# Kernel tuning notes

Measured on AMD Instinct MI355X. Metric: run time of the kernel, lower is better.

Reference implementation:

```python
import jax, jax.numpy as jnp
import numpy as np

DT = 0.1
THRESH = 10.0

def setup_inputs() -> dict:
    key = jax.random.key(0)
    ks = jax.random.split(key, 6)
    B, S, H, V = 2, 1024, 1024, 50257
    hidden_states = jax.random.normal(ks[0], (B, S, H), dtype=jnp.float32)
    ttu_state = jnp.zeros((B, 3), dtype=jnp.float32)
    W_imp = jax.random.normal(ks[1], (3, H), dtype=jnp.float32) * 0.02
    b_imp = jnp.zeros((3,), dtype=jnp.float32)
    W_lm = jax.random.normal(ks[2], (V, H), dtype=jnp.float32) * 0.02
    W_mod = jax.random.normal(ks[3], (V, 3), dtype=jnp.float32) * 0.02
    # gamma, alpha_c, beta_c, delta, alpha_d, epsilon, alpha_m
    ttu_params = jax.random.uniform(ks[4], (7,), dtype=jnp.float32, minval=0.1, maxval=1.0)
    return {"hidden_states": hidden_states, "ttu_state": ttu_state,
            "W_imp": W_imp, "b_imp": b_imp, "W_lm": W_lm, "W_mod": W_mod,
            "ttu_params": ttu_params}

def _ttu_scan(ttu_state, impulses, ttu_params):
    # impulses: [S, B, 3] (time-major for scan)
    gamma, alpha_c, beta_c, delta, alpha_d, epsilon, alpha_m = ttu_params
    def step(state, imp):
        phi_c, phi_d, phi_m = state[:, 0], state[:, 1], state[:, 2]
        dphi_c = gamma * imp[:, 0] - alpha_c * phi_c - beta_c * phi_c * phi_d
        dphi_d = delta * phi_c ** 2 - alpha_d * phi_d
        dphi_m = epsilon * phi_d - alpha_m * phi_m
        new_c = phi_c + DT * dphi_c
        new_d = phi_d + DT * dphi_d
        new_m = phi_m + DT * dphi_m
        # saturation damping on phi_d
        new_d = jnp.where(jnp.abs(new_d) > THRESH, jnp.float32(0.5), jnp.float32(1.0)) * new_d
        new_state = jnp.stack([new_c, new_d, new_m], axis=1)  # [B, 3]
        return new_state, new_state
    return jax.lax.scan(step, ttu_state, impulses)

def reference(hidden_states, ttu_state, W_imp, b_imp, W_lm, W_mod, ttu_params):
    # impulse projections computed in batch up front: [S, B, 3]
    impulses = jnp.einsum('bsh,dh->sbd', hidden_states, W_imp) + b_imp
    final_state, states = _ttu_scan(ttu_state, impulses, ttu_params)  # states: [S, B, 3]
    # base lm logits + 0.1 * modulation from ttu trajectory
    logits = jnp.einsum('bsh,vh->bsv', hidden_states, W_lm) \
           + 0.1 * jnp.einsum('sbd,vd->bsv', states, W_mod)
    return logits, final_state
```

## Files before the change

kernel.cpp:

```cpp
#include <hip/hip_runtime.h>
#include <hip/hip_bf16.h>

typedef float  f32x4  __attribute__((ext_vector_type(4)));
typedef short  bf16x8 __attribute__((ext_vector_type(8)));
typedef short  bf16x4 __attribute__((ext_vector_type(4)));

typedef const void __attribute__((address_space(1))) gv_t;
typedef void __attribute__((address_space(3))) sv_t;

namespace {

constexpr int B_ = 2;
constexpr int S_ = 1024;
constexpr int H_ = 1024;
constexpr int V_ = 50257;
constexpr int M_ = B_ * S_;
constexpr int VP2_ = 50432;
constexpr int VP1_ = 50304;
constexpr float DT_ = 0.1f;
constexpr float THRESH_ = 10.0f;

constexpr int BK = 64;
constexpr int NT = H_ / BK;

__device__ __forceinline__ unsigned short f2bf(float f) {
  union { float f; unsigned u; } x;
  x.f = f;
  x.u += 0x7FFFu + ((x.u >> 16) & 1u);
  return (unsigned short)(x.u >> 16);
}

__global__ void cvt_hidden_impulse_kernel(const float* __restrict__ hidden,
                                          const float* __restrict__ W_imp,
                                          const float* __restrict__ b_imp,
                                          unsigned short* __restrict__ hid_bf,
                                          float* __restrict__ imp) {
  const int m = blockIdx.x;
  const int t = threadIdx.x;
  const float4 hv = reinterpret_cast<const float4*>(hidden + (size_t)m * H_)[t];
  const float4 wv = reinterpret_cast<const float4*>(W_imp)[t];
  bf16x4 o;
  o[0] = (short)f2bf(hv.x); o[1] = (short)f2bf(hv.y);
  o[2] = (short)f2bf(hv.z); o[3] = (short)f2bf(hv.w);
  *(bf16x4*)(hid_bf + (size_t)m * H_ + t * 4) = o;
  float p = hv.x * wv.x + hv.y * wv.y + hv.z * wv.z + hv.w * wv.w;
  #pragma unroll
  for (int off = 32; off; off >>= 1) p += __shfl_down(p, off);
  __shared__ float partial[4];
  if ((t & 63) == 0) partial[t >> 6] = p;
  __syncthreads();
  if (t == 0) {
    const float v = partial[0] + partial[1] + partial[2] + partial[3] + b_imp[0];
    const int b = m >> 10;
    const int s = m & (S_ - 1);
    imp[s * B_ + b] = v;
  }
}

__device__ __forceinline__ void scan_body(const float* __restrict__ imp_s,
                                          const float* __restrict__ ttu_state,
                                          const float* __restrict__ ttu_params,
                                          float* __restrict__ states,
                                          float* __restrict__ final_out, int t) {
  if (t < B_) {
    const float gamma   = ttu_params[0];
    const float alpha_c = ttu_params[1];
    const float beta_c  = ttu_params[2];
    const float delta   = ttu_params[3];
    const float alpha_d = ttu_params[4];
    const float epsilon = ttu_params[5];
    const float alpha_m = ttu_params[6];
    float c = ttu_state[t * 3 + 0];
    float d = ttu_state[t * 3 + 1];
    float m = ttu_state[t * 3 + 2];
    for (int s = 0; s < S_; ++s) {
      const float ii = imp_s[s * B_ + t];
      const float dc = gamma * ii - alpha_c * c - beta_c * c * d;
      const float dd = delta * c * c - alpha_d * d;
      const float dm = epsilon * d - alpha_m * m;
      c = c + DT_ * dc;
      float nd = d + DT_ * dd;
      m = m + DT_ * dm;
      nd = (fabsf(nd) > THRESH_ ? 0.5f : 1.0f) * nd;
      d = nd;
      float* st = states + (size_t)(s * B_ + t) * 3;
      st[0] = c; st[1] = d; st[2] = m;
    }
    final_out[t * 3 + 0] = c;
    final_out[t * 3 + 1] = d;
    final_out[t * 3 + 2] = m;
  }
}

__global__ void ttu_scan_kernel(const float* __restrict__ imp,
                                const float* __restrict__ ttu_state,
                                const float* __restrict__ ttu_params,
                                float* __restrict__ states,
                                float* __restrict__ final_out) {
  __shared__ float imp_s[S_ * B_];
  const int t = threadIdx.x;
  for (int i = t; i < S_ * B_; i += 64) imp_s[i] = imp[i];
  __syncthreads();
  scan_body(imp_s, ttu_state, ttu_params, states, final_out, t);
}

__global__ void cvt_wlm_scan_kernel(const float* __restrict__ src,
                                    unsigned short* __restrict__ dst,
                                    long n_src, long n_dst,
                                    const float* __restrict__ imp,
                                    const float* __restrict__ ttu_state,
                                    const float* __restrict__ ttu_params,
                                    float* __restrict__ states,
                                    float* __restrict__ final_out) {
  __shared__ float imp_s[S_ * B_];
  const int t = threadIdx.x;
  if (blockIdx.x == gridDim.x - 1) {
    for (int i = t; i < S_ * B_; i += 256) imp_s[i] = imp[i];
    __syncthreads();
    scan_body(imp_s, ttu_state, ttu_params, states, final_out, t);
    return;
  }
  const long stride = (long)(gridDim.x - 1) * blockDim.x * 8;
  for (long i = ((long)blockIdx.x * blockDim.x + t) * 8; i < n_dst; i += stride) {
    bf16x8 v;
    if (i < n_src) {
      const float4 a = *(const float4*)(src + i);
      const float4 b = *(const float4*)(src + i + 4);
      v[0] = (short)f2bf(a.x); v[1] = (short)f2bf(a.y);
      v[2] = (short)f2bf(a.z); v[3] = (short)f2bf(a.w);
      v[4] = (short)f2bf(b.x); v[5] = (short)f2bf(b.y);
      v[6] = (short)f2bf(b.z); v[7] = (short)f2bf(b.w);
    } else {
      v = (bf16x8){0, 0, 0, 0, 0, 0, 0, 0};
    }
    *(bf16x8*)(dst + i) = v;
  }
}

__global__ void cvt_bf16_kernel(const float* __restrict__ src,
                                unsigned short* __restrict__ dst,
                                long n_src, long n_dst) {
  const long stride = (long)gridDim.x * blockDim.x * 8;
  for (long i = ((long)blockIdx.x * blockDim.x + threadIdx.x) * 8; i < n_dst; i += stride) {
    bf16x8 v;
    if (i < n_src) {
      const float4 a = *(const float4*)(src + i);
      const float4 b = *(const float4*)(src + i + 4);
      v[0] = (short)f2bf(a.x); v[1] = (short)f2bf(a.y);
      v[2] = (short)f2bf(a.z); v[3] = (short)f2bf(a.w);
      v[4] = (short)f2bf(b.x); v[5] = (short)f2bf(b.y);
      v[6] = (short)f2bf(b.z); v[7] = (short)f2bf(b.w);
    } else {
      v = (bf16x8){0, 0, 0, 0, 0, 0, 0, 0};
    }
    *(bf16x8*)(dst + i) = v;
  }
}

__global__ __launch_bounds__(512, 2) void ttu_gemm_bf16_256v2_kernel(
    const unsigned short* __restrict__ Ab,
    const unsigned short* __restrict__ Bb,
    const float* __restrict__ states,
    const float* __restrict__ Wmod,
    float* __restrict__ out)
{
  __shared__ unsigned short A_s[2][256 * BK];
  __shared__ unsigned short B_s[2][256 * BK];
  __shared__ float st_s[256][3];
  __shared__ float wm_s[256][3];

  const int t = threadIdx.x;
  const int cpx = gridDim.x >> 3;
  const int bid = (blockIdx.x & 7) * cpx + (blockIdx.x >> 3);
  const int mb = bid & 7;
  const int nb = bid >> 3;
  const int m0 = mb * 256;
  const int n0 = nb * 256;

  if (t < 256) {
    const int m = m0 + t;
    const int b = m >> 10;
    const int s = m & (S_ - 1);
    const float* st = states + (size_t)(s * B_ + b) * 3;
    st_s[t][0] = st[0]; st_s[t][1] = st[1]; st_s[t][2] = st[2];
  } else {
    const int tt = t - 256;
    const int n = n0 + tt;
    const bool ok = n < V_;
    wm_s[tt][0] = ok ? Wmod[n * 3 + 0] : 0.f;
    wm_s[tt][1] = ok ? Wmod[n * 3 + 1] : 0.f;
    wm_s[tt][2] = ok ? Wmod[n * 3 + 2] : 0.f;
  }

  const int lane = t & 63;
  const int wid  = t >> 6;
  const int lr   = lane >> 3;
  const int ch   = lane & 7;
  const int wmi  = wid >> 2;
  const int wni  = wid & 3;
  const int lm   = lane & 15;
  const int kg   = lane >> 4;

  const unsigned short* Abase = Ab + (size_t)m0 * H_;
  const unsigned short* Bbase = Bb + (size_t)n0 * H_;

  auto STAGE_ALL = [&](int buf, int kt) {
    const int k0 = kt * BK;
    #pragma unroll
    for (int h = 0; h < 4; ++h) {
      const unsigned short* gb = (h < 2) ? Abase : Bbase;
      unsigned short* ls = (h < 2) ? &A_s[buf][0] : &B_s[buf][0];
      const int half = (h & 1) * 128;
      #pragma unroll
      for (int n = 0; n < 2; ++n) {
        const int rbase = half + wid * 16 + n * 8;
        const int r  = rbase + lr;
        const int sc = ch ^ (r & 7);
        __builtin_amdgcn_global_load_lds(
            (gv_t*)(gb + (size_t)r * H_ + k0 + sc * 8),
            (sv_t*)(ls + rbase * BK), 16, 0, 0);
      }
    }
  };

  f32x4 acc[8][4];
  #pragma unroll
  for (int i = 0; i < 8; ++i)
    #pragma unroll
    for (int j = 0; j < 4; ++j)
      acc[i][j] = (f32x4){0.f, 0.f, 0.f, 0.f};

  STAGE_ALL(0, 0);

  int cur = 0;
  for (int kt = 0; kt < NT; ++kt) {
    const int nxt = cur ^ 1;
    asm volatile("s_barrier" ::: "memory");
    if (kt + 1 < NT) {
      STAGE_ALL(nxt, kt + 1);
      asm volatile("s_waitcnt vmcnt(8)" ::: "memory");
    } else {
      asm volatile("s_waitcnt vmcnt(0)" ::: "memory");
    }
    asm volatile("s_barrier" ::: "memory");

    const unsigned short* As = &A_s[cur][0];
    const unsigned short* Bs = &B_s[cur][0];

    bf16x8 bfr[4][2];
    #pragma unroll
    for (int j = 0; j < 4; ++j)
      #pragma unroll
      for (int ks = 0; ks < 2; ++ks) {
        const int r = wni * 64 + j * 16 + lm;
        bfr[j][ks] = *(const bf16x8*)&Bs[r * BK + (((ks * 4 + kg) ^ (r & 7)) << 3)];
      }
    bf16x8 af[2][2][2];
    #pragma unroll
    for (int i2 = 0; i2 < 2; ++i2)
      #pragma unroll
      for (int ks = 0; ks < 2; ++ks) {
        const int r = wmi * 128 + i2 * 16 + lm;
        af[0][i2][ks] = *(const bf16x8*)&As[r * BK + (((ks * 4 + kg) ^ (r & 7)) << 3)];
      }
    #pragma unroll
    for (int q = 0; q < 4; ++q) {
      if (q < 3) {
        #pragma unroll
        for (int i2 = 0; i2 < 2; ++i2)
          #pragma unroll
          for (int ks = 0; ks < 2; ++ks) {
            const int r = wmi * 128 + ((q + 1) * 2 + i2) * 16 + lm;
            af[(q + 1) & 1][i2][ks] =
                *(const bf16x8*)&As[r * BK + (((ks * 4 + kg) ^ (r & 7)) << 3)];
          }
      }
      __builtin_amdgcn_s_setprio(1);
      #pragma unroll
      for (int ks = 0; ks < 2; ++ks)
        #pragma unroll
        for (int i2 = 0; i2 < 2; ++i2)
          #pragma unroll
          for (int j = 0; j < 4; ++j)
            acc[q * 2 + i2][j] = __builtin_amdgcn_mfma_f32_16x16x32_bf16(
                af[q & 1][i2][ks], bfr[j][ks], acc[q * 2 + i2][j], 0, 0, 0);
      __builtin_amdgcn_s_setprio(0);
    }
    cur ^= 1;
  }

  #pragma unroll
  for (int i = 0; i < 8; ++i) {
    #pragma unroll
    for (int rr = 0; rr < 4; ++rr) {
      const int mloc = wmi * 128 + i * 16 + kg * 4 + rr;
      const float s0 = st_s[mloc][0], s1 = st_s[mloc][1], s2 = st_s[mloc][2];
      float* orow = out + (size_t)(m0 + mloc) * V_ + n0;
      #pragma unroll
      for (int j = 0; j < 4; ++j) {
        const int nloc = wni * 64 + j * 16 + lm;
        if (n0 + nloc < V_) {
          const float corr = 0.1f * (s0 * wm_s[nloc][0] + s1 * wm_s[nloc][1] + s2 * wm_s[nloc][2]);
          orow[nloc] = acc[i][j][rr] + corr;
        }
      }
    }
  }
}

__global__ __launch_bounds__(256) void ttu_gemm_bf16_db_kernel(
    const unsigned short* __restrict__ Ab,
    const unsigned short* __restrict__ Bb,
    const float* __restrict__ states,
    const float* __restrict__ Wmod,
    float* __restrict__ out)
{
  __shared__ unsigned short AB_s[2][2][128 * BK];
  __shared__ float st_s[128][3];
  __shared__ float wm_s[128][3];

  const int t = threadIdx.x;
  const int cpx = gridDim.x >> 3;
  const int bid = (blockIdx.x & 7) * cpx + (blockIdx.x >> 3);
  const int mb = bid & 15;
  const int nb = bid >> 4;
  const int m0 = mb * 128;
  const int n0 = nb * 128;

  if (t < 128) {
    const int m = m0 + t;
    const int b = m >> 10;
    const int s = m & (S_ - 1);
    const float* st = states + (size_t)(s * B_ + b) * 3;
    st_s[t][0] = st[0]; st_s[t][1] = st[1]; st_s[t][2] = st[2];
  } else {
    const int tt = t - 128;
    const int n = n0 + tt;
    const bool ok = n < V_;
    wm_s[tt][0] = ok ? Wmod[n * 3 + 0] : 0.f;
    wm_s[tt][1] = ok ? Wmod[n * 3 + 1] : 0.f;
    wm_s[tt][2] = ok ? Wmod[n * 3 + 2] : 0.f;
  }

  const int lane = t & 63;
  const int wid  = t >> 6;
  const int lr   = lane >> 3;
  const int ch   = lane & 7;
  const int wm   = wid >> 1;
  const int wn   = wid & 1;
  const int lm   = lane & 15;
  const int kg   = lane >> 4;

  const unsigned short* Abase = Ab + (size_t)m0 * H_;
  const unsigned short* Bbase = Bb + (size_t)n0 * H_;
  const int r0 = wid * 32;

  auto STAGE = [&](unsigned short* As, unsigned short* Bs, int kt) {
    const int k0 = kt * BK;
    #pragma unroll
    for (int ins = 0; ins < 4; ++ins) {
      const int lrow = r0 + ins * 8 + lr;
      const int sch  = ch ^ (lrow & 7);
      __builtin_amdgcn_global_load_lds(
          (gv_t*)(Abase + (size_t)lrow * H_ + k0 + sch * 8),
          (sv_t*)(As + (r0 + ins * 8) * BK), 16, 0, 0);
    }
    #pragma unroll
    for (int ins = 0; ins < 4; ++ins) {
      const int lrow = r0 + ins * 8 + lr;
      const int sch  = ch ^ (lrow & 7);
      __builtin_amdgcn_global_load_lds(
          (gv_t*)(Bbase + (size_t)lrow * H_ + k0 + sch * 8),
          (sv_t*)(Bs + (r0 + ins * 8) * BK), 16, 0, 0);
    }
  };

  f32x4 acc[4][4];
  #pragma unroll
  for (int i = 0; i < 4; ++i)
    #pragma unroll
    for (int j = 0; j < 4; ++j)
      acc[i][j] = (f32x4){0.f, 0.f, 0.f, 0.f};

  unsigned short* Ac = &AB_s[0][0][0];
  unsigned short* Bc = &AB_s[0][1][0];
  unsigned short* An = &AB_s[1][0][0];
  unsigned short* Bn = &AB_s[1][1][0];

  STAGE(Ac, Bc, 0);
  __syncthreads();

  for (int kt = 0; kt < NT; ++kt) {
    if (kt + 1 < NT) STAGE(An, Bn, kt + 1);
    bf16x8 af[4][2], bfr[4][2];
    #pragma unroll
    for (int i = 0; i < 4; ++i) {
      const int arow = wm * 64 + i * 16 + lm;
      const int brow = wn * 64 + i * 16 + lm;
      #pragma unroll
      for (int ks = 0; ks < 2; ++ks) {
        af[i][ks]  = *(const bf16x8*)&Ac[arow * BK + (((ks * 4 + kg) ^ (arow & 7)) << 3)];
        bfr[i][ks] = *(const bf16x8*)&Bc[brow * BK + (((ks * 4 + kg) ^ (brow & 7)) << 3)];
      }
    }
    #pragma unroll
    for (int ks = 0; ks < 2; ++ks)
      #pragma unroll
      for (int i = 0; i < 4; ++i)
        #pragma unroll
        for (int j = 0; j < 4; ++j)
          acc[i][j] = __builtin_amdgcn_mfma_f32_16x16x32_bf16(af[i][ks], bfr[j][ks], acc[i][j], 0, 0, 0);
    __syncthreads();
    unsigned short* tp;
    tp = Ac; Ac = An; An = tp;
    tp = Bc; Bc = Bn; Bn = tp;
  }

  #pragma unroll
  for (int i = 0; i < 4; ++i) {
    #pragma unroll
    for (int rr = 0; rr < 4; ++rr) {
      const int mloc = wm * 64 + i * 16 + kg * 4 + rr;
      const float s0 = st_s[mloc][0], s1 = st_s[mloc][1], s2 = st_s[mloc][2];
      float* orow = out + (size_t)(m0 + mloc) * V_ + n0;
      #pragma unroll
      for (int j = 0; j < 4; ++j) {
        const int nloc = wn * 64 + j * 16 + lm;
        if (n0 + nloc < V_) {
          const float corr = 0.1f * (s0 * wm_s[nloc][0] + s1 * wm_s[nloc][1] + s2 * wm_s[nloc][2]);
          orow[nloc] = acc[i][j][rr] + corr;
        }
      }
    }
  }
}

__global__ __launch_bounds__(256) void ttu_gemm_kernel(
    const float* __restrict__ Ag, const float* __restrict__ Bg,
    const float* __restrict__ states, const float* __restrict__ Wmod,
    float* __restrict__ out)
{
  __shared__ unsigned short A_s[128][40];
  __shared__ unsigned short B_s[128][40];
  __shared__ float st_s[128][3];
  __shared__ float wm_s[128][3];

  const int t   = threadIdx.x;
  const int bid = blockIdx.x;
  const int mb  = bid & 15;
  const int nb  = bid >> 4;
  const int m0  = mb * 128;
  const int n0  = nb * 128;

  if (t < 128) {
    const int m = m0 + t;
    const int b = m >> 10;
    const int s = m & (S_ - 1);
    const float* st = states + (size_t)(s * B_ + b) * 3;
    st_s[t][0] = st[0]; st_s[t][1] = st[1]; st_s[t][2] = st[2];
  } else {
    const int tt = t - 128;
    const int n  = n0 + tt;
    const bool ok = n < V_;
    wm_s[tt][0] = ok ? Wmod[n * 3 + 0] : 0.f;
    wm_s[tt][1] = ok ? Wmod[n * 3 + 1] : 0.f;
    wm_s[tt][2] = ok ? Wmod[n * 3 + 2] : 0.f;
  }

  const int r   = t >> 1;
  const int seg = t & 1;
  const float* arow = Ag + (size_t)(m0 + r) * H_ + seg * 16;
  const int  vrow = n0 + r;
  const bool bok  = vrow < V_;
  const float* brow = Bg + (size_t)(bok ? vrow : 0) * H_ + seg * 16;

  const int lane = t & 63;
  const int wid  = t >> 6;
  const int wm   = wid >> 1;
  const int wn   = wid & 1;
  const int lm   = lane & 15;
  const int kg   = lane >> 4;

  f32x4 acc[4][4];
  #pragma unroll
  for (int i = 0; i < 4; ++i)
    #pragma unroll
    for (int j = 0; j < 4; ++j)
      acc[i][j] = (f32x4){0.f, 0.f, 0.f, 0.f};

  for (int kt = 0; kt < H_ / 32; ++kt) {
    const int k0 = kt * 32;
    const float4 av0 = *(const float4*)(arow + k0 + 0);
    const float4 av1 = *(const float4*)(arow + k0 + 4);
    const float4 av2 = *(const float4*)(arow + k0 + 8);
    const float4 av3 = *(const float4*)(arow + k0 + 12);
    float4 bv0 = {0,0,0,0}, bv1 = {0,0,0,0}, bv2 = {0,0,0,0}, bv3 = {0,0,0,0};
    if (bok) {
      bv0 = *(const float4*)(brow + k0 + 0);
      bv1 = *(const float4*)(brow + k0 + 4);
      bv2 = *(const float4*)(brow + k0 + 8);
      bv3 = *(const float4*)(brow + k0 + 12);
    }
    __syncthreads();
    #define CVT4(v) (bf16x4){(short)f2bf((v).x), (short)f2bf((v).y), (short)f2bf((v).z), (short)f2bf((v).w)}
    *(bf16x4*)&A_s[r][seg * 16 + 0]  = CVT4(av0);
    *(bf16x4*)&A_s[r][seg * 16 + 4]  = CVT4(av1);
    *(bf16x4*)&A_s[r][seg * 16 + 8]  = CVT4(av2);
    *(bf16x4*)&A_s[r][seg * 16 + 12] = CVT4(av3);
    *(bf16x4*)&B_s[r][seg * 16 + 0]  = CVT4(bv0);
    *(bf16x4*)&B_s[r][seg * 16 + 4]  = CVT4(bv1);
    *(bf16x4*)&B_s[r][seg * 16 + 8]  = CVT4(bv2);
    *(bf16x4*)&B_s[r][seg * 16 + 12] = CVT4(bv3);
    #undef CVT4
    __syncthreads();
    bf16x8 af[4], bf[4];
    #pragma unroll
    for (int i = 0; i < 4; ++i) {
      af[i] = *(const bf16x8*)&A_s[wm * 64 + i * 16 + lm][kg * 8];
      bf[i] = *(const bf16x8*)&B_s[wn * 64 + i * 16 + lm][kg * 8];
    }
    #pragma unroll
    for (int i = 0; i < 4; ++i)
      #pragma unroll
      for (int j = 0; j < 4; ++j)
        acc[i][j] = __builtin_amdgcn_mfma_f32_16x16x32_bf16(af[i], bf[j], acc[i][j], 0, 0, 0);
  }

  #pragma unroll
  for (int i = 0; i < 4; ++i) {
    #pragma unroll
    for (int rr = 0; rr < 4; ++rr) {
      const int mloc = wm * 64 + i * 16 + kg * 4 + rr;
      const float s0 = st_s[mloc][0], s1 = st_s[mloc][1], s2 = st_s[mloc][2];
      float* orow = out + (size_t)(m0 + mloc) * V_ + n0;
      #pragma unroll
      for (int j = 0; j < 4; ++j) {
        const int nloc = wn * 64 + j * 16 + lm;
        if (n0 + nloc < V_) {
          const float corr = 0.1f * (s0 * wm_s[nloc][0] + s1 * wm_s[nloc][1] + s2 * wm_s[nloc][2]);
          orow[nloc] = acc[i][j][rr] + corr;
        }
      }
    }
  }
}

}

extern "C" void kernel_launch(void* const* d_in, const int* in_sizes, int n_in,
                              void* d_out, int out_size, void* d_ws, size_t ws_size,
                              hipStream_t stream) {
  const float* hidden     = (const float*)d_in[0];
  const float* ttu_state  = (const float*)d_in[1];
  const float* W_imp      = (const float*)d_in[2];
  const float* b_imp      = (const float*)d_in[3];
  const float* W_lm       = (const float*)d_in[4];
  const float* W_mod      = (const float*)d_in[5];
  const float* ttu_params = (const float*)d_in[6];
  float* out = (float*)d_out;

  float* imp    = (float*)d_ws;
  float* states = imp + S_ * B_;
  float* final_out = out + (size_t)B_ * S_ * V_;

  const size_t need256 = 32768 + (size_t)M_ * H_ * 2 + (size_t)VP2_ * H_ * 2;
  const size_t need128 = 32768 + (size_t)M_ * H_ * 2 + (size_t)VP1_ * H_ * 2;

  if (ws_size >= need256) {
    unsigned short* hid_bf = (unsigned short*)((char*)d_ws + 32768);
    unsigned short* wlm_bf = hid_bf + (size_t)M_ * H_;
    cvt_hidden_impulse_kernel<<<M_, 256, 0, stream>>>(hidden, W_imp, b_imp, hid_bf, imp);
    cvt_wlm_scan_kernel<<<4097, 256, 0, stream>>>(W_lm, wlm_bf,
                                                  (long)V_ * H_, (long)VP2_ * H_,
                                                  imp, ttu_state, ttu_params,
                                                  states, final_out);
    const int grid = (VP2_ / 256) * (M_ / 256);
    ttu_gemm_bf16_256v2_kernel<<<grid, 512, 0, stream>>>(hid_bf, wlm_bf, states, W_mod, out);
  } else if (ws_size >= need128) {
    unsigned short* hid_bf = (unsigned short*)((char*)d_ws + 32768);
    unsigned short* wlm_bf = hid_bf + (size_t)M_ * H_;
    cvt_hidden_impulse_kernel<<<M_, 256, 0, stream>>>(hidden, W_imp, b_imp, hid_bf, imp);
    ttu_scan_kernel<<<1, 64, 0, stream>>>(imp, ttu_state, ttu_params, states, final_out);
    cvt_bf16_kernel<<<4096, 256, 0, stream>>>(W_lm, wlm_bf, (long)V_ * H_, (long)VP1_ * H_);
    const int grid = (VP1_ / 128) * (M_ / 128);
    ttu_gemm_bf16_db_kernel<<<grid, 256, 0, stream>>>(hid_bf, wlm_bf, states, W_mod, out);
  } else {
    cvt_hidden_impulse_kernel<<<M_, 256, 0, stream>>>(hidden, W_imp, b_imp,
                                                      (unsigned short*)d_ws, imp);
    ttu_scan_kernel<<<1, 64, 0, stream>>>(imp, ttu_state, ttu_params, states, final_out);
    const int grid = ((V_ + 127) / 128) * (M_ / 128);
    ttu_gemm_kernel<<<grid, 256, 0, stream>>>(hidden, W_lm, states, W_mod, out);
  }
}
```

Baseline: 483.6 us.

## Switch 256x256 bf16 GEMM to 4-stage BK=32 LDS pipeline

The main GEMM kernel goes from a double-buffered BK=64 tile to a four-buffer ring with BK=32. Three k-slices stay in flight, with matching vmcnt waits and a new XOR swizzle for the narrower rows. The aim is to hide global-to-LDS latency better while keeping LDS use about the same (4x32 instead of 2x64). In exchange there are twice as many barrier pairs per K, and each iteration does half the MFMA work. The convert/scan kernel's grid is also halved, which changes how many blocks handle the W_lm conversion alongside the scan.

```diff
diff --git a/kernel.cpp b/kernel.cpp
--- a/kernel.cpp
+++ b/kernel.cpp
@@ -22,6 +22,8 @@
 
 constexpr int BK = 64;
 constexpr int NT = H_ / BK;
+constexpr int BK2 = 32;
+constexpr int NT2 = H_ / BK2;
 
 __device__ __forceinline__ unsigned short f2bf(float f) {
   union { float f; unsigned u; } x;
@@ -157,15 +159,15 @@
   }
 }
 
-__global__ __launch_bounds__(512, 2) void ttu_gemm_bf16_256v2_kernel(
+__global__ __launch_bounds__(512, 2) void ttu_gemm_bf16_256v3_kernel(
     const unsigned short* __restrict__ Ab,
     const unsigned short* __restrict__ Bb,
     const float* __restrict__ states,
     const float* __restrict__ Wmod,
     float* __restrict__ out)
 {
-  __shared__ unsigned short A_s[2][256 * BK];
-  __shared__ unsigned short B_s[2][256 * BK];
+  __shared__ unsigned short A_s[4][256 * BK2];
+  __shared__ unsigned short B_s[4][256 * BK2];
   __shared__ float st_s[256][3];
   __shared__ float wm_s[256][3];
 
@@ -194,8 +196,8 @@
 
   const int lane = t & 63;
   const int wid  = t >> 6;
-  const int lr   = lane >> 3;
-  const int ch   = lane & 7;
+  const int lr   = lane >> 2;
+  const int ch   = lane & 3;
   const int wmi  = wid >> 2;
   const int wni  = wid & 3;
   const int lm   = lane & 15;
@@ -204,21 +206,20 @@
   const unsigned short* Abase = Ab + (size_t)m0 * H_;
   const unsigned short* Bbase = Bb + (size_t)n0 * H_;
 
-  auto STAGE_ALL = [&](int buf, int kt) {
-    const int k0 = kt * BK;
-    #pragma unroll
-    for (int h = 0; h < 4; ++h) {
-      const unsigned short* gb = (h < 2) ? Abase : Bbase;
-      unsigned short* ls = (h < 2) ? &A_s[buf][0] : &B_s[buf][0];
-      const int half = (h & 1) * 128;
+  auto STAGE = [&](int buf, int kt) {
+    const int k0 = kt * BK2;
+    #pragma unroll
+    for (int h = 0; h < 2; ++h) {
+      const unsigned short* gb = h ? Bbase : Abase;
+      unsigned short* ls = h ? &B_s[buf][0] : &A_s[buf][0];
       #pragma unroll
       for (int n = 0; n < 2; ++n) {
-        const int rbase = half + wid * 16 + n * 8;
+        const int rbase = wid * 32 + n * 16;
         const int r  = rbase + lr;
-        const int sc = ch ^ (r & 7);
+        const int sc = ch ^ ((r >> 1) & 3);
         __builtin_amdgcn_global_load_lds(
             (gv_t*)(gb + (size_t)r * H_ + k0 + sc * 8),
-            (sv_t*)(ls + rbase * BK), 16, 0, 0);
+            (sv_t*)(ls + rbase * BK2), 16, 0, 0);
       }
     }
   };
@@ -230,63 +231,59 @@
     for (int j = 0; j < 4; ++j)
       acc[i][j] = (f32x4){0.f, 0.f, 0.f, 0.f};
 
-  STAGE_ALL(0, 0);
-
-  int cur = 0;
-  for (int kt = 0; kt < NT; ++kt) {
-    const int nxt = cur ^ 1;
+  STAGE(0, 0);
+  STAGE(1, 1);
+  STAGE(2, 2);
+
+  for (int kt = 0; kt < NT2; ++kt) {
     asm volatile("s_barrier" ::: "memory");
-    if (kt + 1 < NT) {
-      STAGE_ALL(nxt, kt + 1);
+    const int rem = NT2 - 1 - kt;
+    if (rem >= 3) {
+      STAGE((kt + 3) & 3, kt + 3);
+      asm volatile("s_waitcnt vmcnt(12)" ::: "memory");
+    } else if (rem == 2) {
       asm volatile("s_waitcnt vmcnt(8)" ::: "memory");
+    } else if (rem == 1) {
+      asm volatile("s_waitcnt vmcnt(4)" ::: "memory");
     } else {
       asm volatile("s_waitcnt vmcnt(0)" ::: "memory");
     }
     asm volatile("s_barrier" ::: "memory");
 
-    const unsigned short* As = &A_s[cur][0];
-    const unsigned short* Bs = &B_s[cur][0];
-
-    bf16x8 bfr[4][2];
-    #pragma unroll
-    for (int j = 0; j < 4; ++j)
-      #pragma unroll
-      for (int ks = 0; ks < 2; ++ks) {
-        const int r = wni * 64 + j * 16 + lm;
-        bfr[j][ks] = *(const bf16x8*)&Bs[r * BK + (((ks * 4 + kg) ^ (r & 7)) << 3)];
-      }
-    bf16x8 af[2][2][2];
-    #pragma unroll
-    for (int i2 = 0; i2 < 2; ++i2)
-      #pragma unroll
-      for (int ks = 0; ks < 2; ++ks) {
-        const int r = wmi * 128 + i2 * 16 + lm;
-        af[0][i2][ks] = *(const bf16x8*)&As[r * BK + (((ks * 4 + kg) ^ (r & 7)) << 3)];
-      }
+    const unsigned short* As = &A_s[kt & 3][0];
+    const unsigned short* Bs = &B_s[kt & 3][0];
+
+    bf16x8 bfr[4];
+    #pragma unroll
+    for (int j = 0; j < 4; ++j) {
+      const int r = wni * 64 + j * 16 + lm;
+      bfr[j] = *(const bf16x8*)&Bs[r * BK2 + ((kg ^ ((r >> 1) & 3)) << 3)];
+    }
+    bf16x8 af[2][2];
+    #pragma unroll
+    for (int i2 = 0; i2 < 2; ++i2) {
+      const int r = wmi * 128 + i2 * 16 + lm;
+      af[0][i2] = *(const bf16x8*)&As[r * BK2 + ((kg ^ ((r >> 1) & 3)) << 3)];
+    }
     #pragma unroll
     for (int q = 0; q < 4; ++q) {
       if (q < 3) {
         #pragma unroll
-        for (int i2 = 0; i2 < 2; ++i2)
-          #pragma unroll
-          for (int ks = 0; ks < 2; ++ks) {
-            const int r = wmi * 128 + ((q + 1) * 2 + i2) * 16 + lm;
-            af[(q + 1) & 1][i2][ks] =
-                *(const bf16x8*)&As[r * BK + (((ks * 4 + kg) ^ (r & 7)) << 3)];
-          }
+        for (int i2 = 0; i2 < 2; ++i2) {
+          const int r = wmi * 128 + ((q + 1) * 2 + i2) * 16 + lm;
+          af[(q + 1) & 1][i2] =
+              *(const bf16x8*)&As[r * BK2 + ((kg ^ ((r >> 1) & 3)) << 3)];
+        }
       }
       __builtin_amdgcn_s_setprio(1);
       #pragma unroll
-      for (int ks = 0; ks < 2; ++ks)
+      for (int i2 = 0; i2 < 2; ++i2)
         #pragma unroll
-        for (int i2 = 0; i2 < 2; ++i2)
-          #pragma unroll
-          for (int j = 0; j < 4; ++j)
-            acc[q * 2 + i2][j] = __builtin_amdgcn_mfma_f32_16x16x32_bf16(
-                af[q & 1][i2][ks], bfr[j][ks], acc[q * 2 + i2][j], 0, 0, 0);
+        for (int j = 0; j < 4; ++j)
+          acc[q * 2 + i2][j] = __builtin_amdgcn_mfma_f32_16x16x32_bf16(
+              af[q & 1][i2], bfr[j], acc[q * 2 + i2][j], 0, 0, 0);
       __builtin_amdgcn_s_setprio(0);
     }
-    cur ^= 1;
   }
 
   #pragma unroll
@@ -570,12 +567,12 @@
     unsigned short* hid_bf = (unsigned short*)((char*)d_ws + 32768);
     unsigned short* wlm_bf = hid_bf + (size_t)M_ * H_;
     cvt_hidden_impulse_kernel<<<M_, 256, 0, stream>>>(hidden, W_imp, b_imp, hid_bf, imp);
-    cvt_wlm_scan_kernel<<<4097, 256, 0, stream>>>(W_lm, wlm_bf,
+    cvt_wlm_scan_kernel<<<2049, 256, 0, stream>>>(W_lm, wlm_bf,
                                                   (long)V_ * H_, (long)VP2_ * H_,
                                                   imp, ttu_state, ttu_params,
                                                   states, final_out);
     const int grid = (VP2_ / 256) * (M_ / 256);
-    ttu_gemm_bf16_256v2_kernel<<<grid, 512, 0, stream>>>(hid_bf, wlm_bf, states, W_mod, out);
+    ttu_gemm_bf16_256v3_kernel<<<grid, 512, 0, stream>>>(hid_bf, wlm_bf, states, W_mod, out);
   } else if (ws_size >= need128) {
     unsigned short* hid_bf = (unsigned short*)((char*)d_ws + 32768);
     unsigned short* wlm_bf = hid_bf + (size_t)M_ * H_;
```

New measurement: 513.1 us. 1.06x slower.
